# Kernel tuning notes

Hardware: AMD Instinct MI355X
Metric: run time of the kernel (lower is better)

The kernel has to match this reference:

```python
import jax, jax.numpy as jnp
import numpy as np
import math

HIDDEN = 2048
NUM_HEADS = 16
HEAD_DIM = HIDDEN // NUM_HEADS
B, S = 2, 2048


def setup_inputs() -> dict:
    key = jax.random.key(0)
    k1, k2, k3, k4, k5 = jax.random.split(key, 5)
    scale = 1.0 / math.sqrt(HIDDEN)
    return {
        "hidden_states": jax.random.normal(k1, (B, S, HIDDEN), dtype=jnp.float32),
        "attention_mask": jnp.ones((B, S), dtype=jnp.float32),
        "Wq": jax.random.normal(k2, (HIDDEN, HIDDEN), dtype=jnp.float32) * scale,
        "Wk": jax.random.normal(k3, (HEAD_DIM, HIDDEN), dtype=jnp.float32) * scale,
        "Wv": jax.random.normal(k4, (HEAD_DIM, HIDDEN), dtype=jnp.float32) * scale,
        "Wo": jax.random.normal(k5, (HIDDEN, HIDDEN), dtype=jnp.float32) * scale,
    }


def reference(hidden_states, attention_mask, Wq, Wk, Wv, Wo):
    bsz, tgt, _ = hidden_states.shape
    # projections (torch Linear: x @ W.T)
    q = (hidden_states @ Wq.T).reshape(bsz, tgt, NUM_HEADS, HEAD_DIM).transpose(0, 2, 1, 3)  # [B,H,S,D]
    k = (hidden_states @ Wk.T)[:, None, :, :]  # [B,1,S,D] (MQA single KV head)
    v = (hidden_states @ Wv.T)[:, None, :, :]
    # scores with MQA broadcast (no K expand materialization)
    scores = jnp.einsum("bhsd,bokd->bhsk", q, k) / math.sqrt(HEAD_DIM)  # [B,H,S,S]
    neg = jnp.finfo(scores.dtype).min
    scores = scores + (1.0 - attention_mask)[:, None, None, :] * neg
    probs = jax.nn.softmax(scores, axis=-1)
    attn = jnp.einsum("bhsk,bokd->bhsd", probs, v)  # [B,H,S,D]
    out = attn.transpose(0, 2, 1, 3).reshape(bsz, tgt, HIDDEN) @ Wo.T
    # cache returned by the module (expanded to all heads, as in torch code)
    key_states = jnp.broadcast_to(k, (bsz, NUM_HEADS, tgt, HEAD_DIM))
    value_states = jnp.broadcast_to(v, (bsz, NUM_HEADS, tgt, HEAD_DIM))
    return out, key_states, value_states
```

## Files before the change

kernel.cpp:

```cpp
#include <hip/hip_runtime.h>
#include <hip/hip_bf16.h>
#include <math.h>

#define B_   2
#define S_   2048
#define HID  2048
#define NH   16
#define HD   128

typedef __bf16 bf16_t;
typedef __bf16 bf16x4 __attribute__((ext_vector_type(4)));
typedef __bf16 bf16x8 __attribute__((ext_vector_type(8)));
typedef float  f32x4  __attribute__((ext_vector_type(4)));
typedef unsigned int u32x4 __attribute__((ext_vector_type(4)));

__device__ __forceinline__ f32x4 mfma16(bf16x8 a, bf16x8 b, f32x4 c) {
    return __builtin_amdgcn_mfma_f32_16x16x32_bf16(a, b, c, 0, 0, 0);
}

__device__ __forceinline__ void gl2lds16(const void* g, void* l) {
    __builtin_amdgcn_global_load_lds((__attribute__((address_space(1))) void*)(g),
                                     (__attribute__((address_space(3))) void*)(l),
                                     16, 0, 0);
}

__device__ __forceinline__ unsigned int pkbf(float a, float b) {
    unsigned short ua = __builtin_bit_cast(unsigned short, (bf16_t)a);
    unsigned short ub = __builtin_bit_cast(unsigned short, (bf16_t)b);
    return (unsigned int)ua | ((unsigned int)ub << 16);
}

__global__ void convert_bf16(const float* __restrict__ s0, const float* __restrict__ s1,
                             const float* __restrict__ s2, const float* __restrict__ s3,
                             const float* __restrict__ s4,
                             bf16_t* __restrict__ d0, bf16_t* __restrict__ d1,
                             bf16_t* __restrict__ d2, bf16_t* __restrict__ d3,
                             bf16_t* __restrict__ d4)
{
    const size_t stride = (size_t)gridDim.x * blockDim.x;
    for (size_t i = (size_t)blockIdx.x * blockDim.x + threadIdx.x; i < 4325376; i += stride) {
        const float* s; bf16_t* d; size_t off;
        if (i < 2097152)      { s = s0; d = d0; off = i; }
        else if (i < 3145728) { s = s1; d = d1; off = i - 2097152; }
        else if (i < 3211264) { s = s2; d = d2; off = i - 3145728; }
        else if (i < 3276800) { s = s3; d = d3; off = i - 3211264; }
        else                  { s = s4; d = d4; off = i - 3276800; }
        float4 v = ((const float4*)s)[off];
        bf16x4 o;
        o[0] = (bf16_t)v.x; o[1] = (bf16_t)v.y; o[2] = (bf16_t)v.z; o[3] = (bf16_t)v.w;
        ((bf16x4*)d)[off] = o;
    }
}

__global__ void broadcast_kv(const bf16_t* __restrict__ k_ws, const bf16_t* __restrict__ v_ws,
                             float* __restrict__ keyo, float* __restrict__ valo)
{
    const size_t stride = (size_t)gridDim.x * blockDim.x;
    for (size_t i = (size_t)blockIdx.x * blockDim.x + threadIdx.x; i < 4194304; i += stride) {
        int which = i >= 2097152;
        size_t f = which ? i - 2097152 : i;
        size_t e = f * 4;
        int d = (int)(e & 127);
        size_t s = (e >> 7) & 2047;
        size_t b = e >> 22;
        const bf16_t* src = (which ? v_ws : k_ws) + (b * S_ + s) * HD + d;
        bf16x4 kv = *(const bf16x4*)src;
        float4 o;
        o.x = (float)kv[0]; o.y = (float)kv[1]; o.z = (float)kv[2]; o.w = (float)kv[3];
        *(float4*)((which ? valo : keyo) + e) = o;
    }
}

template <int MODE>
__global__ __launch_bounds__(256, 2)
void gemm_nt(const bf16_t* __restrict__ A,  const bf16_t* __restrict__ B0,
             const bf16_t* __restrict__ B1, const bf16_t* __restrict__ B2,
             bf16_t* __restrict__ q_ws, bf16_t* __restrict__ k_ws,
             bf16_t* __restrict__ v_ws, bf16_t* __restrict__ vt_ws,
             float* __restrict__ outf)
{
    __shared__ __align__(16) ushort sA[128 * 32];
    __shared__ __align__(16) ushort sB[128 * 32];

    const int tid  = threadIdx.x;
    const int lane = tid & 63;
    const int wave = tid >> 6;
    const int quad = lane >> 4;
    const int l16  = lane & 15;
    const int bn = blockIdx.x, bm = blockIdx.y;
    const int wm = (wave & 1) * 64;
    const int wn = (wave >> 1) * 64;

    const bf16_t* Bbase;
    if (MODE == 0) Bbase = (bn < 16) ? (B0 + (size_t)bn * 128 * HID) : (bn == 16 ? B1 : B2);
    else           Bbase = B0 + (size_t)bn * 128 * HID;
    const bf16_t* Abase = A + (size_t)bm * 128 * HID;

    const int c0 = tid, c1 = tid + 256;
    const int r0 = c0 >> 2, o0 = (c0 & 3) * 8;
    const int r1 = c1 >> 2, o1 = (c1 & 3) * 8;

    f32x4 acc[4][4] = {};

    for (int kt = 0; kt < HID / 32; ++kt) {
        const int ko = kt * 32;
        gl2lds16(Abase + (size_t)r0 * HID + ko + o0, sA + c0 * 8);
        gl2lds16(Abase + (size_t)r1 * HID + ko + o1, sA + c1 * 8);
        gl2lds16(Bbase + (size_t)r0 * HID + ko + o0, sB + c0 * 8);
        gl2lds16(Bbase + (size_t)r1 * HID + ko + o1, sB + c1 * 8);
        __syncthreads();

        bf16x8 af[4], bfr[4];
        for (int mt = 0; mt < 4; ++mt)
            af[mt] = *(const bf16x8*)(sA + (wm + mt * 16 + l16) * 32 + quad * 8);
        for (int nt = 0; nt < 4; ++nt)
            bfr[nt] = *(const bf16x8*)(sB + (wn + nt * 16 + l16) * 32 + quad * 8);
        for (int mt = 0; mt < 4; ++mt)
            for (int nt = 0; nt < 4; ++nt)
                acc[mt][nt] = mfma16(af[mt], bfr[nt], acc[mt][nt]);
        __syncthreads();
    }

    for (int mt = 0; mt < 4; ++mt) {
        for (int nt = 0; nt < 4; ++nt) {
            for (int j = 0; j < 4; ++j) {
                float v = acc[mt][nt][j];
                int row = bm * 128 + wm + mt * 16 + quad * 4 + j;
                int col = wn + nt * 16 + l16;
                if (MODE == 1) {
                    outf[(size_t)row * HID + bn * 128 + col] = v;
                } else {
                    bf16_t bv = (bf16_t)v;
                    if (bn < 16) {
                        q_ws[(size_t)row * HID + bn * 128 + col] = bv;
                    } else {
                        int b = row >> 11, s = row & 2047, d = col;
                        if (bn == 16) {
                            k_ws[((size_t)b * S_ + s) * HD + d] = bv;
                        } else {
                            v_ws[((size_t)b * S_ + s) * HD + d] = bv;
                            vt_ws[((size_t)b * HD + d) * S_ + s] = bv;
                        }
                    }
                }
            }
        }
    }
}

#define SV_U 8192
#define SM_U 16384

__global__ __launch_bounds__(256, 2)
void attn_kernel(const bf16_t* __restrict__ Qw, const bf16_t* __restrict__ Kc,
                 const bf16_t* __restrict__ Vt, const float* __restrict__ mask,
                 bf16_t* __restrict__ Ow)
{
    __shared__ __align__(16) ushort smem[16512];
    float* sMask = (float*)&smem[SM_U];

    const int tid  = threadIdx.x;
    const int lane = tid & 63;
    const int wave = tid >> 6;
    const int quad = lane >> 4;
    const int l16  = lane & 15;
    const int qt = blockIdx.x;
    const int bh = blockIdx.y;
    const int b = bh >> 4, h = bh & 15;

    const bf16_t* kg = Kc + (size_t)b * S_ * HD;
    const bf16_t* vg = Vt + (size_t)b * HD * S_;

    bf16x8 qf[2][4];
    {
        const bf16_t* qg = Qw + ((size_t)(b * S_ + qt * 128 + wave * 32)) * HID + h * HD;
#pragma unroll
        for (int mt = 0; mt < 2; ++mt)
#pragma unroll
            for (int kk = 0; kk < 4; ++kk)
                qf[mt][kk] = *(const bf16x8*)(qg + (size_t)(mt * 16 + l16) * HID + kk * 32 + quad * 8);
    }

    f32x4 oa[2][8] = {};
    float mrow[2] = { -INFINITY, -INFINITY };
    float lrow[2] = { 0.f, 0.f };

    const float scale2 = 0.08838834764831845f * 1.4426950408889634f;
    const float NEGF   = -3.4028234663852886e38f;
    const float LOG2E  = 1.4426950408889634f;

    for (int kt = 0; kt < S_ / 64; ++kt) {
        __syncthreads();
        {
            uint4 kr[4], vr[4];
#pragma unroll
            for (int i = 0; i < 4; ++i) {
                int c = tid + i * 256;
                kr[i] = *(const uint4*)(kg + (size_t)(kt * 64 + (c >> 4)) * HD + (c & 15) * 8);
                vr[i] = *(const uint4*)(vg + (size_t)(c >> 3) * S_ + kt * 64 + (c & 7) * 8);
            }
#pragma unroll
            for (int i = 0; i < 4; ++i) {
                int c = tid + i * 256;
                int krow = c >> 4, kchk = c & 15;
                *(uint4*)(&smem[krow * 128 + ((kchk ^ (krow & 7)) << 3)]) = kr[i];
                int vrow = c >> 3, vchk = c & 7;
                *(uint4*)(&smem[SV_U + vrow * 64 + ((vchk ^ (vrow & 7)) << 3)]) = vr[i];
            }
        }
        if (tid < 64) {
            float mv = mask[b * S_ + kt * 64 + tid];
            sMask[tid] = (1.0f - mv) * NEGF * LOG2E;
        }
        __syncthreads();

        f32x4 sa[2][4] = {};
#pragma unroll
        for (int kk = 0; kk < 4; ++kk)
#pragma unroll
            for (int nt = 0; nt < 4; ++nt) {
                bf16x8 kf = *(const bf16x8*)(&smem[(nt * 16 + l16) * 128 + (((4 * kk + quad) ^ (l16 & 7)) << 3)]);
#pragma unroll
                for (int mt = 0; mt < 2; ++mt)
                    sa[mt][nt] = mfma16(kf, qf[mt][kk], sa[mt][nt]);
            }
#pragma unroll
        for (int nt = 0; nt < 4; ++nt) {
            f32x4 m4 = *(const f32x4*)&sMask[nt * 16 + quad * 4];
#pragma unroll
            for (int mt = 0; mt < 2; ++mt)
#pragma unroll
                for (int j = 0; j < 4; ++j)
                    sa[mt][nt][j] = sa[mt][nt][j] * scale2 + m4[j];
        }

        float rm[2];
#pragma unroll
        for (int mt = 0; mt < 2; ++mt) {
            float m = sa[mt][0][0];
#pragma unroll
            for (int nt = 0; nt < 4; ++nt)
#pragma unroll
                for (int j = 0; j < 4; ++j)
                    m = fmaxf(m, sa[mt][nt][j]);
            m = fmaxf(m, __shfl_xor(m, 16));
            m = fmaxf(m, __shfl_xor(m, 32));
            rm[mt] = m;
        }
        bool need = (rm[0] > mrow[0] + 8.0f) || (rm[1] > mrow[1] + 8.0f);
        if (__any((int)need)) {
#pragma unroll
            for (int mt = 0; mt < 2; ++mt) {
                float mnew  = fmaxf(mrow[mt], rm[mt]);
                float alpha = exp2f(mrow[mt] - mnew);
                mrow[mt] = mnew;
                lrow[mt] *= alpha;
#pragma unroll
                for (int j = 0; j < 4; ++j) {
                    float aj = __shfl(alpha, (lane & 48) | (quad * 4 + j));
#pragma unroll
                    for (int nt = 0; nt < 8; ++nt) oa[mt][nt][j] *= aj;
                }
            }
        }
        unsigned int g[2][4][2];
#pragma unroll
        for (int mt = 0; mt < 2; ++mt) {
            float rs = 0.f;
#pragma unroll
            for (int nt = 0; nt < 4; ++nt) {
                float p0 = exp2f(sa[mt][nt][0] - mrow[mt]);
                float p1 = exp2f(sa[mt][nt][1] - mrow[mt]);
                float p2 = exp2f(sa[mt][nt][2] - mrow[mt]);
                float p3 = exp2f(sa[mt][nt][3] - mrow[mt]);
                rs += (p0 + p1) + (p2 + p3);
                g[mt][nt][0] = pkbf(p0, p1);
                g[mt][nt][1] = pkbf(p2, p3);
            }
            rs += __shfl_xor(rs, 16);
            rs += __shfl_xor(rs, 32);
            lrow[mt] += rs;
        }

        bf16x8 pf[2][2];
        {
            const int sl = ((quad & 1) << 5) + l16;
            const int sh = sl + 16;
            const bool hi = (quad & 2) != 0;
#pragma unroll
            for (int kk = 0; kk < 2; ++kk)
#pragma unroll
                for (int mt = 0; mt < 2; ++mt) {
                    unsigned int a0 = __shfl(g[mt][2 * kk][0], sl);
                    unsigned int a1 = __shfl(g[mt][2 * kk][1], sl);
                    unsigned int b0 = __shfl(g[mt][2 * kk + 1][0], sl);
                    unsigned int b1 = __shfl(g[mt][2 * kk + 1][1], sl);
                    unsigned int c0 = __shfl(g[mt][2 * kk][0], sh);
                    unsigned int c1 = __shfl(g[mt][2 * kk][1], sh);
                    unsigned int d0 = __shfl(g[mt][2 * kk + 1][0], sh);
                    unsigned int d1 = __shfl(g[mt][2 * kk + 1][1], sh);
                    u32x4 w;
                    w[0] = hi ? b0 : a0;
                    w[1] = hi ? b1 : a1;
                    w[2] = hi ? d0 : c0;
                    w[3] = hi ? d1 : c1;
                    pf[mt][kk] = __builtin_bit_cast(bf16x8, w);
                }
        }

#pragma unroll
        for (int kk = 0; kk < 2; ++kk)
#pragma unroll
            for (int nt = 0; nt < 8; ++nt) {
                bf16x8 vf = *(const bf16x8*)(&smem[SV_U + (nt * 16 + l16) * 64 + (((4 * kk + quad) ^ (l16 & 7)) << 3)]);
#pragma unroll
                for (int mt = 0; mt < 2; ++mt)
                    oa[mt][nt] = mfma16(pf[mt][kk], vf, oa[mt][nt]);
            }
    }

#pragma unroll
    for (int mt = 0; mt < 2; ++mt)
#pragma unroll
        for (int j = 0; j < 4; ++j) {
            float lv = __shfl(lrow[mt], (lane & 48) | (quad * 4 + j));
            float inv = 1.0f / lv;
            int s = qt * 128 + wave * 32 + mt * 16 + quad * 4 + j;
#pragma unroll
            for (int nt = 0; nt < 8; ++nt) {
                int d = nt * 16 + l16;
                Ow[((size_t)(b * S_ + s)) * HID + h * HD + d] = (bf16_t)(oa[mt][nt][j] * inv);
            }
        }
}

extern "C" void kernel_launch(void* const* d_in, const int* in_sizes, int n_in,
                              void* d_out, int out_size, void* d_ws, size_t ws_size,
                              hipStream_t stream) {
    const float* hs   = (const float*)d_in[0];
    const float* mask = (const float*)d_in[1];
    const float* Wq   = (const float*)d_in[2];
    const float* Wk   = (const float*)d_in[3];
    const float* Wv   = (const float*)d_in[4];
    const float* Wo   = (const float*)d_in[5];
    float* out = (float*)d_out;

    bf16_t* wqb = (bf16_t*)out;
    bf16_t* wkb = wqb + 4194304;
    bf16_t* wvb = wkb + 262144;
    bf16_t* qb  = (bf16_t*)(out + 8388608);
    bf16_t* wob = (bf16_t*)(out + 12582912);
    bf16_t* hsb = (bf16_t*)(out + 16777216);
    bf16_t* o_ws = hsb;

    bf16_t* k_ws  = (bf16_t*)d_ws;
    bf16_t* v_ws  = k_ws + 524288;
    bf16_t* vt_ws = v_ws + 524288;

    convert_bf16<<<2048, 256, 0, stream>>>(hs, Wq, Wk, Wv, Wo, hsb, wqb, wkb, wvb, wob);
    gemm_nt<0><<<dim3(18, 32), 256, 0, stream>>>(hsb, wqb, wkb, wvb, qb, k_ws, v_ws, vt_ws, nullptr);
    attn_kernel<<<dim3(16, 32), 256, 0, stream>>>(qb, k_ws, vt_ws, mask, o_ws);
    gemm_nt<1><<<dim3(16, 32), 256, 0, stream>>>(o_ws, wob, nullptr, nullptr, nullptr, nullptr, nullptr, nullptr, out);
    broadcast_kv<<<4096, 256, 0, stream>>>(k_ws, v_ws, out + 8388608, out + 16777216);
}
```

Baseline: 422.1 us.

## Load K/V fragments directly from global memory instead of staging through LDS

Drops the shared-memory staging of K, V^T and mask tiles in the attention kernel, along with both per-iteration barriers. Each wave now reads its MFMA operand fragments and mask values straight from global memory, relying on L1/L2 caching to absorb the reuse across the four waves. This removes LDS traffic and synchronisation, but every wave issues its own global loads with no prefetch overlap, so latency may be exposed.

```diff
diff --git a/kernel.cpp b/kernel.cpp
--- a/kernel.cpp
+++ b/kernel.cpp
@@ -148,17 +148,11 @@
     }
 }
 
-#define SV_U 8192
-#define SM_U 16384
-
 __global__ __launch_bounds__(256, 2)
 void attn_kernel(const bf16_t* __restrict__ Qw, const bf16_t* __restrict__ Kc,
                  const bf16_t* __restrict__ Vt, const float* __restrict__ mask,
                  bf16_t* __restrict__ Ow)
 {
-    __shared__ __align__(16) ushort smem[16512];
-    float* sMask = (float*)&smem[SM_U];
-
     const int tid  = threadIdx.x;
     const int lane = tid & 63;
     const int wave = tid >> 6;
@@ -170,6 +164,7 @@
 
     const bf16_t* kg = Kc + (size_t)b * S_ * HD;
     const bf16_t* vg = Vt + (size_t)b * HD * S_;
+    const float*  mg = mask + (size_t)b * S_;
 
     bf16x8 qf[2][4];
     {
@@ -190,48 +185,27 @@
     const float LOG2E  = 1.4426950408889634f;
 
     for (int kt = 0; kt < S_ / 64; ++kt) {
-        __syncthreads();
-        {
-            uint4 kr[4], vr[4];
-#pragma unroll
-            for (int i = 0; i < 4; ++i) {
-                int c = tid + i * 256;
-                kr[i] = *(const uint4*)(kg + (size_t)(kt * 64 + (c >> 4)) * HD + (c & 15) * 8);
-                vr[i] = *(const uint4*)(vg + (size_t)(c >> 3) * S_ + kt * 64 + (c & 7) * 8);
-            }
-#pragma unroll
-            for (int i = 0; i < 4; ++i) {
-                int c = tid + i * 256;
-                int krow = c >> 4, kchk = c & 15;
-                *(uint4*)(&smem[krow * 128 + ((kchk ^ (krow & 7)) << 3)]) = kr[i];
-                int vrow = c >> 3, vchk = c & 7;
-                *(uint4*)(&smem[SV_U + vrow * 64 + ((vchk ^ (vrow & 7)) << 3)]) = vr[i];
-            }
-        }
-        if (tid < 64) {
-            float mv = mask[b * S_ + kt * 64 + tid];
-            sMask[tid] = (1.0f - mv) * NEGF * LOG2E;
-        }
-        __syncthreads();
-
         f32x4 sa[2][4] = {};
+        const bf16_t* kbase = kg + (size_t)kt * 64 * HD;
 #pragma unroll
         for (int kk = 0; kk < 4; ++kk)
 #pragma unroll
             for (int nt = 0; nt < 4; ++nt) {
-                bf16x8 kf = *(const bf16x8*)(&smem[(nt * 16 + l16) * 128 + (((4 * kk + quad) ^ (l16 & 7)) << 3)]);
+                bf16x8 kf = *(const bf16x8*)(kbase + (size_t)(nt * 16 + l16) * HD + kk * 32 + quad * 8);
 #pragma unroll
                 for (int mt = 0; mt < 2; ++mt)
                     sa[mt][nt] = mfma16(kf, qf[mt][kk], sa[mt][nt]);
             }
 #pragma unroll
         for (int nt = 0; nt < 4; ++nt) {
-            f32x4 m4 = *(const f32x4*)&sMask[nt * 16 + quad * 4];
-#pragma unroll
-            for (int mt = 0; mt < 2; ++mt)
-#pragma unroll
-                for (int j = 0; j < 4; ++j)
-                    sa[mt][nt][j] = sa[mt][nt][j] * scale2 + m4[j];
+            f32x4 m4 = *(const f32x4*)(mg + kt * 64 + nt * 16 + quad * 4);
+#pragma unroll
+            for (int j = 0; j < 4; ++j) {
+                float madd = (1.0f - m4[j]) * NEGF * LOG2E;
+#pragma unroll
+                for (int mt = 0; mt < 2; ++mt)
+                    sa[mt][nt][j] = sa[mt][nt][j] * scale2 + madd;
+            }
         }
 
         float rm[2];
@@ -312,7 +286,7 @@
         for (int kk = 0; kk < 2; ++kk)
 #pragma unroll
             for (int nt = 0; nt < 8; ++nt) {
-                bf16x8 vf = *(const bf16x8*)(&smem[SV_U + (nt * 16 + l16) * 64 + (((4 * kk + quad) ^ (l16 & 7)) << 3)]);
+                bf16x8 vf = *(const bf16x8*)(vg + (size_t)(nt * 16 + l16) * S_ + kt * 64 + kk * 32 + quad * 8);
 #pragma unroll
                 for (int mt = 0; mt < 2; ++mt)
                     oa[mt][nt] = mfma16(pf[mt][kk], vf, oa[mt][nt]);
```

Result: slower. 507.2 us (+20.2%).
